# Kernel tuning notes

Hardware: AMD Instinct MI355X
Metric: run time of the kernel (lower is better)

The kernel has to match this reference:

```python
import jax, jax.numpy as jnp
import numpy as np

S, B, D, DV = 2048, 16, 128, 128


def setup_inputs() -> dict:
    key = jax.random.key(0)
    kq, kk, kv = jax.random.split(key, 3)
    return {
        "query": jax.random.normal(kq, (S, B, D), dtype=jnp.float32),
        "key": jax.random.normal(kk, (S, B, D), dtype=jnp.float32),
        "value": jax.random.normal(kv, (S, B, DV), dtype=jnp.float32),
    }


def reference(query, key, value):
    # sim: [B, S_q, S_k]
    d = key.shape[-1]
    sim = jnp.einsum('sbd,tbd->bst', query, key) / jnp.sqrt(jnp.asarray(d, query.dtype))
    # causal mask: disallow attending to future positions (strictly upper triangle)
    sq, sk = sim.shape[-2], sim.shape[-1]
    causal = jnp.tril(jnp.ones((sq, sk), dtype=bool))  # [S_q, S_k]
    sim = jnp.where(causal[None, :, :], sim, -jnp.inf)
    a = jax.nn.softmax(sim, axis=-1)  # dropout omitted (eval mode, p=0)
    # context: [S_q, B, D_v]
    context = jnp.einsum('bst,tbe->sbe', a, value)
    return context
```

## Files before the change

### kernel.cpp

```cpp
#include <hip/hip_runtime.h>
#include <stdint.h>

#define SS 2048
#define BB 16
#define DD 128
#define DVV 128
#define BQ 64
#define BK 32
#define NTILES (SS / BK)
#define TILE_HW 4096

typedef __attribute__((ext_vector_type(8))) short short8;
typedef __attribute__((ext_vector_type(4))) float float4v;

typedef __attribute__((address_space(1))) const void glob_cv;
typedef __attribute__((address_space(3))) void lds_v;

__device__ __forceinline__ short f2bf(float f) {
  union { float f; uint32_t u; } x;
  x.f = f;
  uint32_t r = x.u + 0x7fffu + ((x.u >> 16) & 1u);
  return (short)(r >> 16);
}

__device__ __forceinline__ int kappa(int quad, int j) {
  return (j < 4) ? (quad * 4 + j) : (16 + quad * 4 + (j - 4));
}

__global__ __launch_bounds__(256) void conv_kv(
    const float* __restrict__ kg, const float* __restrict__ vg,
    short* __restrict__ kimg, short* __restrict__ vimg) {
  __shared__ short tile[BK][136];
  const int t = blockIdx.x, b = blockIdx.y;
  const float* src_base = (blockIdx.z == 0) ? kg : vg;
  short* out = ((blockIdx.z == 0) ? kimg : vimg) + ((size_t)(b * NTILES + t)) * TILE_HW;
#pragma unroll
  for (int p = 0; p < 2; ++p) {
    const int ch = threadIdx.x + p * 256;
    const int key = ch >> 4, c = ch & 15;
    const float* src = src_base + ((size_t)(t * BK + key) * BB + b) * DD + c * 8;
    float4v f0 = *(const float4v*)src;
    float4v f1 = *(const float4v*)(src + 4);
    short8 s;
#pragma unroll
    for (int i = 0; i < 4; ++i) { s[i] = f2bf(f0[i]); s[4 + i] = f2bf(f1[i]); }
    *(short8*)&tile[key][c * 8] = s;
  }
  __syncthreads();
#pragma unroll
  for (int p = 0; p < 2; ++p) {
    const int idx = threadIdx.x + p * 256;
    const int j = idx >> 6, quad = (idx >> 4) & 3, mm = idx & 15;
    short8 s;
    if (blockIdx.z == 0) {
      const int ks = j >> 1, half = j & 1;
      s = *(const short8*)&tile[half * 16 + mm][(ks * 4 + quad) * 8];
    } else {
#pragma unroll
      for (int jj = 0; jj < 8; ++jj) s[jj] = tile[kappa(quad, jj)][j * 16 + mm];
    }
    *(short8*)(out + idx * 8) = s;
  }
}

__global__ __launch_bounds__(512) void attn_fwd(
    const float* __restrict__ qg, const short* __restrict__ kimg,
    const short* __restrict__ vimg, float* __restrict__ og) {
  __shared__ __align__(16) char smem_raw[65536];
  short* const sbuf = (short*)smem_raw;

  const int tid  = threadIdx.x;
  const int wave = tid >> 6;
  const int par  = wave >> 2;
  const int qsub = wave & 3;
  const int lane = tid & 63;
  const int m    = lane & 15;
  const int quad = lane >> 4;
  const int bid  = blockIdx.x;
  const int xcd = bid & 7;
  const int j   = bid >> 3;
  const int qt  = (j < 32) ? j : 63 - j;
  const int b   = 2 * xcd + (j >> 5);
  const int qw  = qt * BQ + qsub * 16;
  const int qrow = qw + m;

  const float cscale = 0.08838834764831845f * 1.4426950408889634f;
  short8 qfrag[4];
#pragma unroll
  for (int ks = 0; ks < 4; ++ks) {
    const float* qp = qg + ((size_t)qrow * BB + b) * DD + ks * 32 + quad * 8;
    float4v f0 = *(const float4v*)qp;
    float4v f1 = *(const float4v*)(qp + 4);
    short8 f;
#pragma unroll
    for (int i = 0; i < 4; ++i) { f[i] = f2bf(f0[i] * cscale); f[4 + i] = f2bf(f1[i] * cscale); }
    qfrag[ks] = f;
  }

  float4v oacc[8];
#pragma unroll
  for (int i = 0; i < 8; ++i) oacc[i] = (float4v){0.f, 0.f, 0.f, 0.f};
  float psum = 0.f;

  const short* kbase = kimg + (size_t)b * NTILES * TILE_HW;
  const short* vbase = vimg + (size_t)b * NTILES * TILE_HW;
  const int cbase = qsub * 4;
  const short* timg = (cbase < 8) ? kbase : vbase;
  const int coff = cbase & 7;
  short* const gbuf0 = sbuf + par * 8192;
  short* const gbuf1 = sbuf + 16384 + par * 8192;

  const int nround = qt + 1;

  {
    const short* src = timg + (size_t)par * TILE_HW + coff * 512 + lane * 8;
#pragma unroll
    for (int c = 0; c < 4; ++c)
      __builtin_amdgcn_global_load_lds((glob_cv*)(src + c * 512),
                                       (lds_v*)&gbuf0[(cbase + c) * 512], 16, 0, 0);
  }
  __syncthreads();

  for (int r = 0; r < nround; ++r) {
    short* const cbuf = (r & 1) ? gbuf1 : gbuf0;
    short* const nbuf = (r & 1) ? gbuf0 : gbuf1;

    if (r + 1 < nround) {
      const int tn = 2 * (r + 1) + par;
      const short* src = timg + (size_t)tn * TILE_HW + coff * 512 + lane * 8;
#pragma unroll
      for (int c = 0; c < 4; ++c)
        __builtin_amdgcn_global_load_lds((glob_cv*)(src + c * 512),
                                         (lds_v*)&nbuf[(cbase + c) * 512], 16, 0, 0);
    }

    const int t = 2 * r + par;
    const short* kb = cbuf;
    const short* vb = cbuf + 8 * 512;

    float4v s0 = {0.f, 0.f, 0.f, 0.f}, s1 = {0.f, 0.f, 0.f, 0.f};
#pragma unroll
    for (int ks = 0; ks < 4; ++ks) {
      short8 kf0 = *(const short8*)(kb + (ks * 2 + 0) * 512 + lane * 8);
      short8 kf1 = *(const short8*)(kb + (ks * 2 + 1) * 512 + lane * 8);
      s0 = __builtin_amdgcn_mfma_f32_16x16x32_bf16(kf0, qfrag[ks], s0, 0, 0, 0);
      s1 = __builtin_amdgcn_mfma_f32_16x16x32_bf16(kf1, qfrag[ks], s1, 0, 0, 0);
    }
    float sv[8];
#pragma unroll
    for (int rr = 0; rr < 4; ++rr) { sv[rr] = s0[rr]; sv[4 + rr] = s1[rr]; }

    const int kt0 = t * BK;
    if (kt0 + BK - 1 > qw) {
#pragma unroll
      for (int jj = 0; jj < 8; ++jj)
        if (kt0 + kappa(quad, jj) > qrow) sv[jj] = -1e30f;
    }

    union { short8 s8; uint32_t w[4]; } pf;
#pragma unroll
    for (int jp = 0; jp < 4; ++jp) {
      float p0 = exp2f(sv[2 * jp]);
      float p1 = exp2f(sv[2 * jp + 1]);
      uint32_t w;
      asm("v_cvt_pk_bf16_f32 %0, %1, %2" : "=v"(w) : "v"(p0), "v"(p1));
      pf.w[jp] = w;
      union { uint32_t u; float f; } lo, hi;
      lo.u = w << 16;
      hi.u = w & 0xffff0000u;
      psum += lo.f;
      psum += hi.f;
    }
    const short8 pfrag = pf.s8;

#pragma unroll
    for (int nt = 0; nt < 8; ++nt) {
      short8 vf = *(const short8*)(vb + nt * 512 + lane * 8);
      oacc[nt] = __builtin_amdgcn_mfma_f32_16x16x32_bf16(pfrag, vf, oacc[nt], 0, 0, 0);
    }

    __syncthreads();
  }

  __syncthreads();
  float* const cw = (float*)smem_raw;
  if (par == 1) {
    float* p = cw + (size_t)(qsub * 64 + lane) * 36;
#pragma unroll
    for (int nt = 0; nt < 8; ++nt) *(float4v*)(p + nt * 4) = oacc[nt];
    p[32] = psum;
  }
  __syncthreads();
  if (par == 0) {
    const float* p = cw + (size_t)(qsub * 64 + lane) * 36;
#pragma unroll
    for (int nt = 0; nt < 8; ++nt) oacc[nt] += *(const float4v*)(p + nt * 4);
    psum += p[32];

    float l = psum;
    l += __shfl_xor(l, 16, 64);
    l += __shfl_xor(l, 32, 64);
    const float linv = 1.0f / l;
    float l4[4];
#pragma unroll
    for (int rr = 0; rr < 4; ++rr) l4[rr] = __shfl(linv, quad * 4 + rr, 64);
#pragma unroll
    for (int rr = 0; rr < 4; ++rr) {
      const int qgl = qw + quad * 4 + rr;
      float* op = og + ((size_t)qgl * BB + b) * DVV + m;
#pragma unroll
      for (int nt = 0; nt < 8; ++nt) op[nt * 16] = oacc[nt][rr] * l4[rr];
    }
  }
}

extern "C" void kernel_launch(void* const* d_in, const int* in_sizes, int n_in,
                              void* d_out, int out_size, void* d_ws, size_t ws_size,
                              hipStream_t stream) {
  const float* q = (const float*)d_in[0];
  const float* k = (const float*)d_in[1];
  const float* v = (const float*)d_in[2];
  float* out = (float*)d_out;
  short* kimg = (short*)d_ws;
  short* vimg = kimg + (size_t)BB * NTILES * TILE_HW;

  conv_kv<<<dim3(NTILES, BB, 2), 256, 0, stream>>>(k, v, kimg, vimg);
  attn_fwd<<<dim3(SS / BQ * BB), 512, 0, stream>>>(q, kimg, vimg, out);
}
```

Measured before the change: 123.2 us.

## Halve waves per block, giving each wave two 16-row query subtiles

After: 133.5 us. 8.4% more time.

```diff
diff --git a/kernel.cpp b/kernel.cpp
--- a/kernel.cpp
+++ b/kernel.cpp
@@ -63,7 +63,7 @@
   }
 }
 
-__global__ __launch_bounds__(512) void attn_fwd(
+__global__ __launch_bounds__(256) void attn_fwd(
     const float* __restrict__ qg, const short* __restrict__ kimg,
     const short* __restrict__ vimg, float* __restrict__ og) {
   __shared__ __align__(16) char smem_raw[65536];
@@ -71,8 +71,8 @@
 
   const int tid  = threadIdx.x;
   const int wave = tid >> 6;
-  const int par  = wave >> 2;
-  const int qsub = wave & 3;
+  const int par  = wave >> 1;
+  const int qsub = wave & 1;
   const int lane = tid & 63;
   const int m    = lane & 15;
   const int quad = lane >> 4;
@@ -81,41 +81,47 @@
   const int j   = bid >> 3;
   const int qt  = (j < 32) ? j : 63 - j;
   const int b   = 2 * xcd + (j >> 5);
-  const int qw  = qt * BQ + qsub * 16;
-  const int qrow = qw + m;
+  const int qw  = qt * BQ + qsub * 32;
+  const int qwB = qw + 16;
 
   const float cscale = 0.08838834764831845f * 1.4426950408889634f;
-  short8 qfrag[4];
+  short8 qfragA[4], qfragB[4];
 #pragma unroll
   for (int ks = 0; ks < 4; ++ks) {
-    const float* qp = qg + ((size_t)qrow * BB + b) * DD + ks * 32 + quad * 8;
-    float4v f0 = *(const float4v*)qp;
-    float4v f1 = *(const float4v*)(qp + 4);
-    short8 f;
-#pragma unroll
-    for (int i = 0; i < 4; ++i) { f[i] = f2bf(f0[i] * cscale); f[4 + i] = f2bf(f1[i] * cscale); }
-    qfrag[ks] = f;
-  }
-
-  float4v oacc[8];
-#pragma unroll
-  for (int i = 0; i < 8; ++i) oacc[i] = (float4v){0.f, 0.f, 0.f, 0.f};
-  float psum = 0.f;
+#pragma unroll
+    for (int sub = 0; sub < 2; ++sub) {
+      const int qrow = qw + sub * 16 + m;
+      const float* qp = qg + ((size_t)qrow * BB + b) * DD + ks * 32 + quad * 8;
+      float4v f0 = *(const float4v*)qp;
+      float4v f1 = *(const float4v*)(qp + 4);
+      short8 f;
+#pragma unroll
+      for (int i = 0; i < 4; ++i) { f[i] = f2bf(f0[i] * cscale); f[4 + i] = f2bf(f1[i] * cscale); }
+      if (sub == 0) qfragA[ks] = f; else qfragB[ks] = f;
+    }
+  }
+
+  float4v oaccA[8], oaccB[8];
+#pragma unroll
+  for (int i = 0; i < 8; ++i) {
+    oaccA[i] = (float4v){0.f, 0.f, 0.f, 0.f};
+    oaccB[i] = (float4v){0.f, 0.f, 0.f, 0.f};
+  }
+  float psumA = 0.f, psumB = 0.f;
 
   const short* kbase = kimg + (size_t)b * NTILES * TILE_HW;
   const short* vbase = vimg + (size_t)b * NTILES * TILE_HW;
-  const int cbase = qsub * 4;
-  const short* timg = (cbase < 8) ? kbase : vbase;
-  const int coff = cbase & 7;
+  const int cbase = qsub * 8;
+  const short* timg = (qsub == 0) ? kbase : vbase;
   short* const gbuf0 = sbuf + par * 8192;
   short* const gbuf1 = sbuf + 16384 + par * 8192;
 
   const int nround = qt + 1;
 
   {
-    const short* src = timg + (size_t)par * TILE_HW + coff * 512 + lane * 8;
-#pragma unroll
-    for (int c = 0; c < 4; ++c)
+    const short* src = timg + (size_t)par * TILE_HW + lane * 8;
+#pragma unroll
+    for (int c = 0; c < 8; ++c)
       __builtin_amdgcn_global_load_lds((glob_cv*)(src + c * 512),
                                        (lds_v*)&gbuf0[(cbase + c) * 512], 16, 0, 0);
   }
@@ -127,9 +133,9 @@
 
     if (r + 1 < nround) {
       const int tn = 2 * (r + 1) + par;
-      const short* src = timg + (size_t)tn * TILE_HW + coff * 512 + lane * 8;
-#pragma unroll
-      for (int c = 0; c < 4; ++c)
+      const short* src = timg + (size_t)tn * TILE_HW + lane * 8;
+#pragma unroll
+      for (int c = 0; c < 8; ++c)
         __builtin_amdgcn_global_load_lds((glob_cv*)(src + c * 512),
                                          (lds_v*)&nbuf[(cbase + c) * 512], 16, 0, 0);
     }
@@ -138,45 +144,70 @@
     const short* kb = cbuf;
     const short* vb = cbuf + 8 * 512;
 
-    float4v s0 = {0.f, 0.f, 0.f, 0.f}, s1 = {0.f, 0.f, 0.f, 0.f};
+    float4v s0A = {0.f, 0.f, 0.f, 0.f}, s1A = {0.f, 0.f, 0.f, 0.f};
+    float4v s0B = {0.f, 0.f, 0.f, 0.f}, s1B = {0.f, 0.f, 0.f, 0.f};
 #pragma unroll
     for (int ks = 0; ks < 4; ++ks) {
       short8 kf0 = *(const short8*)(kb + (ks * 2 + 0) * 512 + lane * 8);
       short8 kf1 = *(const short8*)(kb + (ks * 2 + 1) * 512 + lane * 8);
-      s0 = __builtin_amdgcn_mfma_f32_16x16x32_bf16(kf0, qfrag[ks], s0, 0, 0, 0);
-      s1 = __builtin_amdgcn_mfma_f32_16x16x32_bf16(kf1, qfrag[ks], s1, 0, 0, 0);
-    }
-    float sv[8];
-#pragma unroll
-    for (int rr = 0; rr < 4; ++rr) { sv[rr] = s0[rr]; sv[4 + rr] = s1[rr]; }
+      s0A = __builtin_amdgcn_mfma_f32_16x16x32_bf16(kf0, qfragA[ks], s0A, 0, 0, 0);
+      s1A = __builtin_amdgcn_mfma_f32_16x16x32_bf16(kf1, qfragA[ks], s1A, 0, 0, 0);
+      s0B = __builtin_amdgcn_mfma_f32_16x16x32_bf16(kf0, qfragB[ks], s0B, 0, 0, 0);
+      s1B = __builtin_amdgcn_mfma_f32_16x16x32_bf16(kf1, qfragB[ks], s1B, 0, 0, 0);
+    }
+    float svA[8], svB[8];
+#pragma unroll
+    for (int rr = 0; rr < 4; ++rr) {
+      svA[rr] = s0A[rr]; svA[4 + rr] = s1A[rr];
+      svB[rr] = s0B[rr]; svB[4 + rr] = s1B[rr];
+    }
 
     const int kt0 = t * BK;
     if (kt0 + BK - 1 > qw) {
+      const int qrowA = qw + m;
 #pragma unroll
       for (int jj = 0; jj < 8; ++jj)
-        if (kt0 + kappa(quad, jj) > qrow) sv[jj] = -1e30f;
-    }
-
-    union { short8 s8; uint32_t w[4]; } pf;
+        if (kt0 + kappa(quad, jj) > qrowA) svA[jj] = -1e30f;
+    }
+    if (kt0 + BK - 1 > qwB) {
+      const int qrowB = qwB + m;
+#pragma unroll
+      for (int jj = 0; jj < 8; ++jj)
+        if (kt0 + kappa(quad, jj) > qrowB) svB[jj] = -1e30f;
+    }
+
+    union { short8 s8; uint32_t w[4]; } pfA, pfB;
 #pragma unroll
     for (int jp = 0; jp < 4; ++jp) {
-      float p0 = exp2f(sv[2 * jp]);
-      float p1 = exp2f(sv[2 * jp + 1]);
-      uint32_t w;
-      asm("v_cvt_pk_bf16_f32 %0, %1, %2" : "=v"(w) : "v"(p0), "v"(p1));
-      pf.w[jp] = w;
-      union { uint32_t u; float f; } lo, hi;
-      lo.u = w << 16;
-      hi.u = w & 0xffff0000u;
-      psum += lo.f;
-      psum += hi.f;
-    }
-    const short8 pfrag = pf.s8;
+      {
+        float p0 = exp2f(svA[2 * jp]);
+        float p1 = exp2f(svA[2 * jp + 1]);
+        uint32_t w;
+        asm("v_cvt_pk_bf16_f32 %0, %1, %2" : "=v"(w) : "v"(p0), "v"(p1));
+        pfA.w[jp] = w;
+        union { uint32_t u; float f; } lo, hi;
+        lo.u = w << 16; hi.u = w & 0xffff0000u;
+        psumA += lo.f; psumA += hi.f;
+      }
+      {
+        float p0 = exp2f(svB[2 * jp]);
+        float p1 = exp2f(svB[2 * jp + 1]);
+        uint32_t w;
+        asm("v_cvt_pk_bf16_f32 %0, %1, %2" : "=v"(w) : "v"(p0), "v"(p1));
+        pfB.w[jp] = w;
+        union { uint32_t u; float f; } lo, hi;
+        lo.u = w << 16; hi.u = w & 0xffff0000u;
+        psumB += lo.f; psumB += hi.f;
+      }
+    }
+    const short8 pfragA = pfA.s8;
+    const short8 pfragB = pfB.s8;
 
 #pragma unroll
     for (int nt = 0; nt < 8; ++nt) {
       short8 vf = *(const short8*)(vb + nt * 512 + lane * 8);
-      oacc[nt] = __builtin_amdgcn_mfma_f32_16x16x32_bf16(pfrag, vf, oacc[nt], 0, 0, 0);
+      oaccA[nt] = __builtin_amdgcn_mfma_f32_16x16x32_bf16(pfragA, vf, oaccA[nt], 0, 0, 0);
+      oaccB[nt] = __builtin_amdgcn_mfma_f32_16x16x32_bf16(pfragB, vf, oaccB[nt], 0, 0, 0);
     }
 
     __syncthreads();
@@ -185,31 +216,43 @@
   __syncthreads();
   float* const cw = (float*)smem_raw;
   if (par == 1) {
-    float* p = cw + (size_t)(qsub * 64 + lane) * 36;
-#pragma unroll
-    for (int nt = 0; nt < 8; ++nt) *(float4v*)(p + nt * 4) = oacc[nt];
-    p[32] = psum;
+    float* p = cw + (size_t)(qsub * 64 + lane) * 68;
+#pragma unroll
+    for (int nt = 0; nt < 8; ++nt) {
+      *(float4v*)(p + nt * 4)      = oaccA[nt];
+      *(float4v*)(p + 32 + nt * 4) = oaccB[nt];
+    }
+    p[64] = psumA;
+    p[65] = psumB;
   }
   __syncthreads();
   if (par == 0) {
-    const float* p = cw + (size_t)(qsub * 64 + lane) * 36;
-#pragma unroll
-    for (int nt = 0; nt < 8; ++nt) oacc[nt] += *(const float4v*)(p + nt * 4);
-    psum += p[32];
-
-    float l = psum;
-    l += __shfl_xor(l, 16, 64);
-    l += __shfl_xor(l, 32, 64);
-    const float linv = 1.0f / l;
-    float l4[4];
-#pragma unroll
-    for (int rr = 0; rr < 4; ++rr) l4[rr] = __shfl(linv, quad * 4 + rr, 64);
-#pragma unroll
-    for (int rr = 0; rr < 4; ++rr) {
-      const int qgl = qw + quad * 4 + rr;
-      float* op = og + ((size_t)qgl * BB + b) * DVV + m;
-#pragma unroll
-      for (int nt = 0; nt < 8; ++nt) op[nt * 16] = oacc[nt][rr] * l4[rr];
+    const float* p = cw + (size_t)(qsub * 64 + lane) * 68;
+#pragma unroll
+    for (int nt = 0; nt < 8; ++nt) {
+      oaccA[nt] += *(const float4v*)(p + nt * 4);
+      oaccB[nt] += *(const float4v*)(p + 32 + nt * 4);
+    }
+    psumA += p[64];
+    psumB += p[65];
+
+#pragma unroll
+    for (int sub = 0; sub < 2; ++sub) {
+      float l = (sub == 0) ? psumA : psumB;
+      l += __shfl_xor(l, 16, 64);
+      l += __shfl_xor(l, 32, 64);
+      const float linv = 1.0f / l;
+      float l4[4];
+#pragma unroll
+      for (int rr = 0; rr < 4; ++rr) l4[rr] = __shfl(linv, quad * 4 + rr, 64);
+#pragma unroll
+      for (int rr = 0; rr < 4; ++rr) {
+        const int qgl = qw + sub * 16 + quad * 4 + rr;
+        float* op = og + ((size_t)qgl * BB + b) * DVV + m;
+#pragma unroll
+        for (int nt = 0; nt < 8; ++nt)
+          op[nt * 16] = ((sub == 0) ? oaccA[nt][rr] : oaccB[nt][rr]) * l4[rr];
+      }
     }
   }
 }
@@ -225,5 +268,5 @@
   short* vimg = kimg + (size_t)BB * NTILES * TILE_HW;
 
   conv_kv<<<dim3(NTILES, BB, 2), 256, 0, stream>>>(k, v, kimg, vimg);
-  attn_fwd<<<dim3(SS / BQ * BB), 512, 0, stream>>>(q, kimg, vimg, out);
-}
+  attn_fwd<<<dim3(SS / BQ * BB), 256, 0, stream>>>(q, kimg, vimg, out);
+}
```
